# Kernel tuning notes

Measured on AMD Instinct MI355X. Metric: run time of the kernel, lower is better.

The kernel has to match this reference:

```python
import jax, jax.numpy as jnp
import numpy as np

RGB2GRAY = jnp.array([0.299, 0.587, 0.114], dtype=jnp.float32)

H_IMG, W_IMG = 1080, 1920
NUM, GRID_Y, GRID_X, GRID_W = 1, 16, 16, 8


def _identity_grids(num, grid_y, grid_x, grid_w):
    ident = jnp.array([1., 0, 0, 0, 0, 1., 0, 0, 0, 0, 1., 0], dtype=jnp.float32)
    return jnp.broadcast_to(ident, (num, grid_y, grid_x, grid_w, 12))


def setup_inputs() -> dict:
    key = jax.random.key(0)
    k1, k2 = jax.random.split(key)
    rgb = jax.random.uniform(k1, (3, H_IMG, W_IMG), dtype=jnp.float32)
    # learned grids = identity affine + small perturbation (so slicing is non-trivial)
    grids = _identity_grids(NUM, GRID_Y, GRID_X, GRID_W) \
        + 0.05 * jax.random.normal(k2, (NUM, GRID_Y, GRID_X, GRID_W, 12), dtype=jnp.float32)
    return {"rgb": rgb, "grids": grids, "idx": 0}


def _bilateral_slice(grid, guidance):
    """Trilinear slice. grid: (Hg, Wg, L, 12); guidance: (Hi, Wi) in [0,1].
    Returns (Hi, Wi, 12)."""
    Hg, Wg, L, _ = grid.shape
    Hi, Wi = guidance.shape
    # align_corners-style pixel -> grid coords
    gy = jnp.linspace(0.0, Hg - 1.0, Hi, dtype=jnp.float32)[:, None]   # (Hi,1)
    gx = jnp.linspace(0.0, Wg - 1.0, Wi, dtype=jnp.float32)[None, :]   # (1,Wi)
    gz = jnp.clip(guidance, 0.0, 1.0) * (L - 1.0)                      # (Hi,Wi)

    fy = jnp.floor(gy); wy = gy - fy
    fx = jnp.floor(gx); wx = gx - fx
    fz = jnp.floor(gz); wz = gz - fz
    y0 = jnp.clip(fy.astype(jnp.int32), 0, Hg - 1); y1 = jnp.clip(y0 + 1, 0, Hg - 1)
    x0 = jnp.clip(fx.astype(jnp.int32), 0, Wg - 1); x1 = jnp.clip(x0 + 1, 0, Wg - 1)
    z0 = jnp.clip(fz.astype(jnp.int32), 0, L - 1);  z1 = jnp.clip(z0 + 1, 0, L - 1)

    out = jnp.zeros((Hi, Wi, 12), dtype=grid.dtype)
    for yi, wyi in ((y0, 1.0 - wy), (y1, wy)):
        for xi, wxi in ((x0, 1.0 - wx), (x1, wx)):
            for zi, wzi in ((z0, 1.0 - wz), (z1, wz)):
                w = (wyi * wxi * wzi)[..., None]          # (Hi,Wi,1)
                out = out + grid[yi, xi, zi] * w          # gather -> (Hi,Wi,12)
    return out


def reference(rgb, grids, idx):
    grid = grids[idx]                         # (Hg, Wg, L, 12)
    rgb_hwc = jnp.transpose(rgb, (1, 2, 0))   # (H, W, 3)
    gray = jnp.tensordot(rgb_hwc, RGB2GRAY, axes=([-1], [0]))  # (H, W)
    affine = _bilateral_slice(grid, gray)     # (H, W, 12)
    affine_mat = affine.reshape(-1, 3, 4)     # (H*W, 3, 4)
    rgb_flat = rgb_hwc.reshape(-1, 3)         # (H*W, 3)
    res_rgb = jnp.einsum('nij,nj->ni', affine_mat[..., :3], rgb_flat) + affine_mat[..., 3]
    return (affine_mat, res_rgb)
```

## Files before the change

kernel.cpp:

```cpp
#include <hip/hip_runtime.h>

#define H_IMG 1080
#define W_IMG 1920
#define HW_PIX (H_IMG * W_IMG)
#define GY 16
#define GX 16
#define GL 8
#define CF 12
#define SEG 320

__global__ __launch_bounds__(320) void bg_kernel(
    const float* __restrict__ rgb,
    const float* __restrict__ grids,
    const int* __restrict__ idxp,
    float* __restrict__ out)
{
    __shared__ float4 sg[96];
    __shared__ float  s_aff[SEG * 12];
    __shared__ float  s_res[SEG * 3];

    const int tid = threadIdx.x;
    const int y = blockIdx.y;
    const int xbase = blockIdx.x * SEG;
    const int p0 = y * W_IMG + xbase;
    const int x = xbase + tid;
    const int p = p0 + tid;

    float r = rgb[p];
    float g = rgb[HW_PIX + p];
    float b = rgb[2 * HW_PIX + p];

    const float* grid = grids + (size_t)idxp[0] * (GY * GX * GL * CF);

    float gyv = (float)y * (15.0f / 1079.0f);
    float fy = floorf(gyv);
    float wy = gyv - fy;
    int y0 = min(max((int)fy, 0), GY - 1);
    int y1 = min(y0 + 1, GY - 1);

    int xc0 = (int)floorf((float)xbase * (15.0f / 1919.0f));

    if (tid < 96) {
        int xi  = tid / 24;
        int rem = tid - xi * 24;
        int z   = rem / 3;
        int c4  = rem - z * 3;
        int xc  = min(xc0 + xi, GX - 1);
        const float4* c0 = (const float4*)(grid + (size_t)((y0 * GX + xc) * GL + z) * CF) + c4;
        const float4* c1 = (const float4*)(grid + (size_t)((y1 * GX + xc) * GL + z) * CF) + c4;
        float4 a = *c0, bb = *c1;
        float wy0 = 1.0f - wy;
        float4 rr;
        rr.x = wy0 * a.x + wy * bb.x;
        rr.y = wy0 * a.y + wy * bb.y;
        rr.z = wy0 * a.z + wy * bb.z;
        rr.w = wy0 * a.w + wy * bb.w;
        sg[tid] = rr;
    }
    __syncthreads();

    float gray = 0.299f * r + 0.587f * g + 0.114f * b;

    float gxv = (float)x * (15.0f / 1919.0f);
    float fx = floorf(gxv), wx = gxv - fx;
    float gz = fminf(fmaxf(gray, 0.0f), 1.0f) * 7.0f;
    float fz = floorf(gz), wz = gz - fz;

    int x0g = min(max((int)fx, 0), GX - 1);
    int x1g = min(x0g + 1, GX - 1);
    int xi0 = x0g - xc0;
    int xi1 = x1g - xc0;
    int z0 = min(max((int)fz, 0), GL - 1);
    int z1 = min(z0 + 1, GL - 1);

    float w00 = (1.0f - wx) * (1.0f - wz);
    float w01 = (1.0f - wx) * wz;
    float w10 = wx * (1.0f - wz);
    float w11 = wx * wz;

    const float4* A = sg + (xi0 * 24 + z0 * 3);
    const float4* B = sg + (xi0 * 24 + z1 * 3);
    const float4* C = sg + (xi1 * 24 + z0 * 3);
    const float4* D = sg + (xi1 * 24 + z1 * 3);

    float4 acc[3];
#pragma unroll
    for (int j = 0; j < 3; ++j) {
        float4 va = A[j], vb = B[j], vc = C[j], vd = D[j];
        float4 o;
        o.x = fmaf(w00, va.x, fmaf(w01, vb.x, fmaf(w10, vc.x, w11 * vd.x)));
        o.y = fmaf(w00, va.y, fmaf(w01, vb.y, fmaf(w10, vc.y, w11 * vd.y)));
        o.z = fmaf(w00, va.z, fmaf(w01, vb.z, fmaf(w10, vc.z, w11 * vd.z)));
        o.w = fmaf(w00, va.w, fmaf(w01, vb.w, fmaf(w10, vc.w, w11 * vd.w)));
        acc[j] = o;
    }

    float4* sa = (float4*)(s_aff + tid * 12);
    sa[0] = acc[0];
    sa[1] = acc[1];
    sa[2] = acc[2];

    s_res[tid * 3 + 0] = fmaf(acc[0].x, r, fmaf(acc[0].y, g, fmaf(acc[0].z, b, acc[0].w)));
    s_res[tid * 3 + 1] = fmaf(acc[1].x, r, fmaf(acc[1].y, g, fmaf(acc[1].z, b, acc[1].w)));
    s_res[tid * 3 + 2] = fmaf(acc[2].x, r, fmaf(acc[2].y, g, fmaf(acc[2].z, b, acc[2].w)));

    __syncthreads();

    const float4* sa4 = (const float4*)s_aff;
    float4* ao = (float4*)(out + (size_t)p0 * 12);
    ao[tid]           = sa4[tid];
    ao[tid + SEG]     = sa4[tid + SEG];
    ao[tid + 2 * SEG] = sa4[tid + 2 * SEG];

    if (tid < 240) {
        ((float4*)(out + (size_t)HW_PIX * 12 + (size_t)p0 * 3))[tid] =
            ((const float4*)s_res)[tid];
    }
}

extern "C" void kernel_launch(void* const* d_in, const int* in_sizes, int n_in,
                              void* d_out, int out_size, void* d_ws, size_t ws_size,
                              hipStream_t stream) {
    const float* rgb   = (const float*)d_in[0];
    const float* grids = (const float*)d_in[1];
    const int*   idx   = (const int*)d_in[2];
    float*       out   = (float*)d_out;

    dim3 grid(W_IMG / SEG, H_IMG);
    dim3 block(SEG);
    bg_kernel<<<grid, block, 0, stream>>>(rgb, grids, idx, out);
}
```

Before: 144.9 us.

## Use persistent grid-stride blocks with RGB prefetch and nontemporal stores

Replaces the 6x1080 block grid with 1536 persistent blocks that loop over row segments. Each block loads the next segment's RGB values while it processes the current one, and it writes outputs with nontemporal stores so the streaming writes bypass cache retention. The aim is to hide global load latency and cut block launch overhead in this bandwidth-bound kernel. In exchange, fewer blocks are resident per CU, register pressure rises from the prefetch, and each iteration still carries two barriers.

```diff
diff --git a/kernel.cpp b/kernel.cpp
--- a/kernel.cpp
+++ b/kernel.cpp
@@ -8,8 +8,13 @@
 #define GL 8
 #define CF 12
 #define SEG 320
+#define SPR 6
+#define NSEG (H_IMG * SPR)
+#define NBLK 1536
 
-__global__ __launch_bounds__(320) void bg_kernel(
+typedef float v4f __attribute__((ext_vector_type(4)));
+
+__global__ __launch_bounds__(SEG) void bg_kernel(
     const float* __restrict__ rgb,
     const float* __restrict__ grids,
     const int* __restrict__ idxp,
@@ -20,101 +25,121 @@
     __shared__ float  s_res[SEG * 3];
 
     const int tid = threadIdx.x;
-    const int y = blockIdx.y;
-    const int xbase = blockIdx.x * SEG;
-    const int p0 = y * W_IMG + xbase;
-    const int x = xbase + tid;
-    const int p = p0 + tid;
+    const float* grid = grids + (size_t)idxp[0] * (GY * GX * GL * CF);
 
+    int s = blockIdx.x;
+
+    int y = s / SPR;
+    int xb = (s - y * SPR) * SEG;
+    int p = y * W_IMG + xb + tid;
     float r = rgb[p];
     float g = rgb[HW_PIX + p];
     float b = rgb[2 * HW_PIX + p];
 
-    const float* grid = grids + (size_t)idxp[0] * (GY * GX * GL * CF);
+    while (s < NSEG) {
+        const int snext = s + NBLK;
+        y  = s / SPR;
+        xb = (s - y * SPR) * SEG;
+        const int p0 = y * W_IMG + xb;
+        const int x  = xb + tid;
 
-    float gyv = (float)y * (15.0f / 1079.0f);
-    float fy = floorf(gyv);
-    float wy = gyv - fy;
-    int y0 = min(max((int)fy, 0), GY - 1);
-    int y1 = min(y0 + 1, GY - 1);
+        float gyv = (float)y * (15.0f / 1079.0f);
+        float fy = floorf(gyv);
+        float wy = gyv - fy;
+        int y0 = min(max((int)fy, 0), GY - 1);
+        int y1 = min(y0 + 1, GY - 1);
+        int xc0 = (int)floorf((float)xb * (15.0f / 1919.0f));
 
-    int xc0 = (int)floorf((float)xbase * (15.0f / 1919.0f));
+        if (tid < 96) {
+            int xi  = tid / 24;
+            int rem = tid - xi * 24;
+            int z   = rem / 3;
+            int c4  = rem - z * 3;
+            int xc  = min(xc0 + xi, GX - 1);
+            const float4* c0 = (const float4*)(grid + (size_t)((y0 * GX + xc) * GL + z) * CF) + c4;
+            const float4* c1 = (const float4*)(grid + (size_t)((y1 * GX + xc) * GL + z) * CF) + c4;
+            float4 a = *c0, bb = *c1;
+            float wy0 = 1.0f - wy;
+            float4 rr;
+            rr.x = wy0 * a.x + wy * bb.x;
+            rr.y = wy0 * a.y + wy * bb.y;
+            rr.z = wy0 * a.z + wy * bb.z;
+            rr.w = wy0 * a.w + wy * bb.w;
+            sg[tid] = rr;
+        }
 
-    if (tid < 96) {
-        int xi  = tid / 24;
-        int rem = tid - xi * 24;
-        int z   = rem / 3;
-        int c4  = rem - z * 3;
-        int xc  = min(xc0 + xi, GX - 1);
-        const float4* c0 = (const float4*)(grid + (size_t)((y0 * GX + xc) * GL + z) * CF) + c4;
-        const float4* c1 = (const float4*)(grid + (size_t)((y1 * GX + xc) * GL + z) * CF) + c4;
-        float4 a = *c0, bb = *c1;
-        float wy0 = 1.0f - wy;
-        float4 rr;
-        rr.x = wy0 * a.x + wy * bb.x;
-        rr.y = wy0 * a.y + wy * bb.y;
-        rr.z = wy0 * a.z + wy * bb.z;
-        rr.w = wy0 * a.w + wy * bb.w;
-        sg[tid] = rr;
-    }
-    __syncthreads();
+        float rn = 0.0f, gn = 0.0f, bn = 0.0f;
+        if (snext < NSEG) {
+            int yn  = snext / SPR;
+            int xbn = (snext - yn * SPR) * SEG;
+            int pn  = yn * W_IMG + xbn + tid;
+            rn = rgb[pn];
+            gn = rgb[HW_PIX + pn];
+            bn = rgb[2 * HW_PIX + pn];
+        }
 
-    float gray = 0.299f * r + 0.587f * g + 0.114f * b;
+        __syncthreads();
 
-    float gxv = (float)x * (15.0f / 1919.0f);
-    float fx = floorf(gxv), wx = gxv - fx;
-    float gz = fminf(fmaxf(gray, 0.0f), 1.0f) * 7.0f;
-    float fz = floorf(gz), wz = gz - fz;
+        float gray = 0.299f * r + 0.587f * g + 0.114f * b;
 
-    int x0g = min(max((int)fx, 0), GX - 1);
-    int x1g = min(x0g + 1, GX - 1);
-    int xi0 = x0g - xc0;
-    int xi1 = x1g - xc0;
-    int z0 = min(max((int)fz, 0), GL - 1);
-    int z1 = min(z0 + 1, GL - 1);
+        float gxv = (float)x * (15.0f / 1919.0f);
+        float fx = floorf(gxv), wx = gxv - fx;
+        float gz = fminf(fmaxf(gray, 0.0f), 1.0f) * 7.0f;
+        float fz = floorf(gz), wz = gz - fz;
 
-    float w00 = (1.0f - wx) * (1.0f - wz);
-    float w01 = (1.0f - wx) * wz;
-    float w10 = wx * (1.0f - wz);
-    float w11 = wx * wz;
+        int x0g = min(max((int)fx, 0), GX - 1);
+        int x1g = min(x0g + 1, GX - 1);
+        int xi0 = x0g - xc0;
+        int xi1 = x1g - xc0;
+        int z0 = min(max((int)fz, 0), GL - 1);
+        int z1 = min(z0 + 1, GL - 1);
 
-    const float4* A = sg + (xi0 * 24 + z0 * 3);
-    const float4* B = sg + (xi0 * 24 + z1 * 3);
-    const float4* C = sg + (xi1 * 24 + z0 * 3);
-    const float4* D = sg + (xi1 * 24 + z1 * 3);
+        float w00 = (1.0f - wx) * (1.0f - wz);
+        float w01 = (1.0f - wx) * wz;
+        float w10 = wx * (1.0f - wz);
+        float w11 = wx * wz;
 
-    float4 acc[3];
+        const float4* A = sg + (xi0 * 24 + z0 * 3);
+        const float4* B = sg + (xi0 * 24 + z1 * 3);
+        const float4* C = sg + (xi1 * 24 + z0 * 3);
+        const float4* D = sg + (xi1 * 24 + z1 * 3);
+
+        float4 acc[3];
 #pragma unroll
-    for (int j = 0; j < 3; ++j) {
-        float4 va = A[j], vb = B[j], vc = C[j], vd = D[j];
-        float4 o;
-        o.x = fmaf(w00, va.x, fmaf(w01, vb.x, fmaf(w10, vc.x, w11 * vd.x)));
-        o.y = fmaf(w00, va.y, fmaf(w01, vb.y, fmaf(w10, vc.y, w11 * vd.y)));
-        o.z = fmaf(w00, va.z, fmaf(w01, vb.z, fmaf(w10, vc.z, w11 * vd.z)));
-        o.w = fmaf(w00, va.w, fmaf(w01, vb.w, fmaf(w10, vc.w, w11 * vd.w)));
-        acc[j] = o;
-    }
+        for (int j = 0; j < 3; ++j) {
+            float4 va = A[j], vb = B[j], vc = C[j], vd = D[j];
+            float4 o;
+            o.x = fmaf(w00, va.x, fmaf(w01, vb.x, fmaf(w10, vc.x, w11 * vd.x)));
+            o.y = fmaf(w00, va.y, fmaf(w01, vb.y, fmaf(w10, vc.y, w11 * vd.y)));
+            o.z = fmaf(w00, va.z, fmaf(w01, vb.z, fmaf(w10, vc.z, w11 * vd.z)));
+            o.w = fmaf(w00, va.w, fmaf(w01, vb.w, fmaf(w10, vc.w, w11 * vd.w)));
+            acc[j] = o;
+        }
 
-    float4* sa = (float4*)(s_aff + tid * 12);
-    sa[0] = acc[0];
-    sa[1] = acc[1];
-    sa[2] = acc[2];
+        float4* sa = (float4*)(s_aff + tid * 12);
+        sa[0] = acc[0];
+        sa[1] = acc[1];
+        sa[2] = acc[2];
 
-    s_res[tid * 3 + 0] = fmaf(acc[0].x, r, fmaf(acc[0].y, g, fmaf(acc[0].z, b, acc[0].w)));
-    s_res[tid * 3 + 1] = fmaf(acc[1].x, r, fmaf(acc[1].y, g, fmaf(acc[1].z, b, acc[1].w)));
-    s_res[tid * 3 + 2] = fmaf(acc[2].x, r, fmaf(acc[2].y, g, fmaf(acc[2].z, b, acc[2].w)));
+        s_res[tid * 3 + 0] = fmaf(acc[0].x, r, fmaf(acc[0].y, g, fmaf(acc[0].z, b, acc[0].w)));
+        s_res[tid * 3 + 1] = fmaf(acc[1].x, r, fmaf(acc[1].y, g, fmaf(acc[1].z, b, acc[1].w)));
+        s_res[tid * 3 + 2] = fmaf(acc[2].x, r, fmaf(acc[2].y, g, fmaf(acc[2].z, b, acc[2].w)));
 
-    __syncthreads();
+        __syncthreads();
 
-    const float4* sa4 = (const float4*)s_aff;
-    float4* ao = (float4*)(out + (size_t)p0 * 12);
-    ao[tid]           = sa4[tid];
-    ao[tid + SEG]     = sa4[tid + SEG];
-    ao[tid + 2 * SEG] = sa4[tid + 2 * SEG];
+        const v4f* sa4 = (const v4f*)s_aff;
+        v4f* ao = (v4f*)(out + (size_t)p0 * 12);
+        __builtin_nontemporal_store(sa4[tid],           ao + tid);
+        __builtin_nontemporal_store(sa4[tid + SEG],     ao + tid + SEG);
+        __builtin_nontemporal_store(sa4[tid + 2 * SEG], ao + tid + 2 * SEG);
 
-    if (tid < 240) {
-        ((float4*)(out + (size_t)HW_PIX * 12 + (size_t)p0 * 3))[tid] =
-            ((const float4*)s_res)[tid];
+        if (tid < 240) {
+            v4f* ro = (v4f*)(out + (size_t)HW_PIX * 12 + (size_t)p0 * 3);
+            __builtin_nontemporal_store(((const v4f*)s_res)[tid], ro + tid);
+        }
+
+        r = rn; g = gn; b = bn;
+        s = snext;
     }
 }
 
@@ -126,7 +151,7 @@
     const int*   idx   = (const int*)d_in[2];
     float*       out   = (float*)d_out;
 
-    dim3 grid(W_IMG / SEG, H_IMG);
+    dim3 grid(NBLK);
     dim3 block(SEG);
     bg_kernel<<<grid, block, 0, stream>>>(rgb, grids, idx, out);
 }
```

After: 155.1 us. 1.07x slower.
